# Kernel tuning notes

Measured on AMD Instinct MI355X. Metric: run time of the kernel, lower is better.

The kernel has to match this reference:

```python
import jax, jax.numpy as jnp
import numpy as np

FEAT_DIM = 128
NODE_DIM = 64
BS, C, H, W = 32, 128, 64, 64
TOPK = 4096


def setup_inputs() -> dict:
    key = jax.random.key(0)
    k1, k2, k3, k4, k5, k6 = jax.random.split(key, 6)
    feature_map = jax.random.normal(k1, (BS, C, H, W), dtype=jnp.float32)
    # peak (row, col) coordinates in heatmap/feature space, floats in-range
    rc = jax.random.uniform(k2, (BS, TOPK, 2), dtype=jnp.float32)
    peak_coords = rc * jnp.array([H - 1, W - 1], dtype=jnp.float32)
    s1 = 1.0 / np.sqrt(FEAT_DIM)
    s2 = 1.0 / np.sqrt(NODE_DIM)
    W1 = jax.random.uniform(k3, (FEAT_DIM, NODE_DIM), jnp.float32, -s1, s1)
    b1 = jax.random.uniform(k4, (NODE_DIM,), jnp.float32, -s1, s1)
    W2 = jax.random.uniform(k5, (NODE_DIM, NODE_DIM), jnp.float32, -s2, s2)
    b2 = jax.random.uniform(k6, (NODE_DIM,), jnp.float32, -s2, s2)
    return {"feature_map": feature_map, "peak_coords": peak_coords,
            "W1": W1, "b1": b1, "W2": W2, "b2": b2}


def _bilinear_gather(feature_map, peak_coords):
    # feature_map: (bs, C, H, W); peak_coords: (bs, topk, 2) as (row, col)
    # Equivalent to F.grid_sample(mode='bilinear', align_corners=True) at
    # grid built from coords normalized by (H-1)/(W-1): the normalization
    # round-trips, so we sample directly at pixel coords (y, x).
    bs, c, h, w = feature_map.shape
    fm = jnp.transpose(feature_map, (0, 2, 3, 1))  # (bs, H, W, C)
    y = peak_coords[..., 0]
    x = peak_coords[..., 1]
    y0 = jnp.floor(y)
    x0 = jnp.floor(x)
    ty = y - y0
    tx = x - x0
    y0i = jnp.clip(y0.astype(jnp.int32), 0, h - 1)
    x0i = jnp.clip(x0.astype(jnp.int32), 0, w - 1)
    y1i = jnp.clip(y0i + 1, 0, h - 1)
    x1i = jnp.clip(x0i + 1, 0, w - 1)
    b = jnp.arange(bs, dtype=jnp.int32)[:, None]  # (bs, 1)
    v00 = fm[b, y0i, x0i]  # (bs, topk, C)
    v01 = fm[b, y0i, x1i]
    v10 = fm[b, y1i, x0i]
    v11 = fm[b, y1i, x1i]
    ty = ty[..., None]
    tx = tx[..., None]
    top = v00 * (1 - tx) + v01 * tx
    bot = v10 * (1 - tx) + v11 * tx
    return top * (1 - ty) + bot * ty  # (bs, topk, C)


def reference(feature_map, peak_coords, W1, b1, W2, b2):
    sampled = _bilinear_gather(feature_map, peak_coords)  # (bs, topk, C)
    h = jax.nn.relu(jnp.einsum('btc,cd->btd', sampled, W1) + b1)
    e = jnp.einsum('btd,de->bte', h, W2) + b2  # (bs, topk, node_dim)
    norm = jnp.linalg.norm(e, axis=-1, keepdims=True)
    return e / jnp.maximum(norm, 1e-12)
```

## Files before the change

kernel.cpp:

```cpp
#include <hip/hip_runtime.h>

#define Hh 64
#define Ww 64
#define Cc 128
#define ND 64
#define BSz 32
#define TOPK 4096
#define HW (Hh * Ww)
#define NPX (BSz * HW)

typedef short bf16x8 __attribute__((ext_vector_type(8)));
typedef unsigned short u16x8 __attribute__((ext_vector_type(8)));
typedef float f32x4 __attribute__((ext_vector_type(4)));

static __device__ __forceinline__ unsigned short f2bf(float f) {
    unsigned int u = __builtin_bit_cast(unsigned int, f);
    u += 0x7fffu + ((u >> 16) & 1u);
    return (unsigned short)(u >> 16);
}
static __device__ __forceinline__ float bf2f(unsigned short s) {
    unsigned int u = ((unsigned int)s) << 16;
    return __builtin_bit_cast(float, u);
}

__global__ void k_prep(const float* __restrict__ W1, const float* __restrict__ W2,
                       unsigned short* __restrict__ w1p, unsigned short* __restrict__ w2p) {
    const int t = threadIdx.x;
#pragma unroll
    for (int k = 0; k < 32; ++k) {
        int i = t + 256 * k;
        int j = i & 7, l = (i >> 3) & 63, kk = (i >> 9) & 3, nt = i >> 11;
        int c = kk * 32 + 8 * (l >> 4) + j, n = nt * 16 + (l & 15);
        w1p[i] = f2bf(W1[c * ND + n]);
    }
#pragma unroll
    for (int k = 0; k < 16; ++k) {
        int i = t + 256 * k;
        int j = i & 7, l = (i >> 3) & 63, kk = (i >> 9) & 1, nt = (i >> 10) & 3;
        int c = kk * 32 + 8 * (l >> 4) + j, n = nt * 16 + (l & 15);
        w2p[i] = f2bf(W2[c * ND + n]);
    }
}

__global__ __launch_bounds__(256) void k_mlp1(const float* __restrict__ fm,
                                              const unsigned short* __restrict__ w1p,
                                              unsigned short* __restrict__ U) {
    __shared__ __align__(16) unsigned short w1s[8192];
    const int t = threadIdx.x;
#pragma unroll
    for (int k = 0; k < 4; ++k) {
        int i = t + 256 * k;
        *(u16x8*)&w1s[i * 8] = *(const u16x8*)&w1p[i * 8];
    }
    __syncthreads();

    const int bid = blockIdx.x;
    const int swz = (bid & 7) * 128 + (bid >> 3);
    const int lane = t & 63, wv = t >> 6;
    const int g = lane >> 4, mr = lane & 15;
    const int p0  = swz * 128 + wv * 32;
    const int b   = p0 >> 12;
    const int pin = p0 & 4095;
    const float* fb = fm + (size_t)b * (Cc * HW);

    bf16x8 aF[2][4];
#pragma unroll
    for (int half = 0; half < 2; ++half) {
        const int px = pin + half * 16 + mr;
#pragma unroll
        for (int kk = 0; kk < 4; ++kk) {
            float v[8];
#pragma unroll
            for (int j = 0; j < 8; ++j)
                v[j] = fb[(size_t)(kk * 32 + 8 * g + j) * HW + px];
            u16x8 o;
#pragma unroll
            for (int j = 0; j < 8; ++j) o[j] = f2bf(v[j]);
            aF[half][kk] = __builtin_bit_cast(bf16x8, o);
        }
    }

    f32x4 acc[2][4];
#pragma unroll
    for (int mt = 0; mt < 2; ++mt)
#pragma unroll
        for (int nt = 0; nt < 4; ++nt) acc[mt][nt] = (f32x4){0.f, 0.f, 0.f, 0.f};

#pragma unroll
    for (int kk = 0; kk < 4; ++kk)
#pragma unroll
        for (int nt = 0; nt < 4; ++nt) {
            bf16x8 bF = *(const bf16x8*)&w1s[((nt * 4 + kk) * 64 + lane) * 8];
            acc[0][nt] = __builtin_amdgcn_mfma_f32_16x16x32_bf16(aF[0][kk], bF, acc[0][nt], 0, 0, 0);
            acc[1][nt] = __builtin_amdgcn_mfma_f32_16x16x32_bf16(aF[1][kk], bF, acc[1][nt], 0, 0, 0);
        }

#pragma unroll
    for (int mt = 0; mt < 2; ++mt)
#pragma unroll
        for (int nt = 0; nt < 4; ++nt)
#pragma unroll
            for (int r = 0; r < 4; ++r) {
                const int row = p0 + mt * 16 + 4 * g + r;
                U[(size_t)row * ND + nt * 16 + mr] = f2bf(acc[mt][nt][r]);
            }
}

__global__ __launch_bounds__(256) void k_fused2(const unsigned short* __restrict__ U,
                                                const float* __restrict__ pc,
                                                const unsigned short* __restrict__ w2p,
                                                const float* __restrict__ b1,
                                                const float* __restrict__ b2,
                                                float* __restrict__ out) {
    __shared__ __align__(16) unsigned short w2s[4096];
    __shared__ __align__(16) float b1s[64];
    __shared__ __align__(16) float b2s[64];
    const int t = threadIdx.x;
#pragma unroll
    for (int k = 0; k < 2; ++k) {
        int i = t + 256 * k;
        *(u16x8*)&w2s[i * 8] = *(const u16x8*)&w2p[i * 8];
    }
    if (t < 64) { b1s[t] = b1[t]; b2s[t] = b2[t]; }
    __syncthreads();

    const int bid = blockIdx.x;
    const int swz = (bid & 7) * 256 + (bid >> 3);
    const int lane = t & 63, wv = t >> 6;
    const int g = lane >> 4, mr = lane & 15;
    const int m0 = swz * 64 + wv * 16;
    const int sm = m0 + mr;

    const float y = pc[2 * (size_t)sm + 0];
    const float x = pc[2 * (size_t)sm + 1];
    const float yf = floorf(y), xf = floorf(x);
    const float ty = y - yf, tx = x - xf;
    int y0 = min(max((int)yf, 0), Hh - 1);
    int x0 = min(max((int)xf, 0), Ww - 1);
    int y1 = min(y0 + 1, Hh - 1);
    int x1 = min(x0 + 1, Ww - 1);
    const float w00 = (1.f - ty) * (1.f - tx), w01 = (1.f - ty) * tx;
    const float w10 = ty * (1.f - tx),         w11 = ty * tx;
    const int bb = sm >> 12;
    const unsigned short* Ub = U + (size_t)bb * (HW * ND) + 8 * g;
    const u16x8* q00 = (const u16x8*)(Ub + (y0 * Ww + x0) * ND);
    const u16x8* q01 = (const u16x8*)(Ub + (y0 * Ww + x1) * ND);
    const u16x8* q10 = (const u16x8*)(Ub + (y1 * Ww + x0) * ND);
    const u16x8* q11 = (const u16x8*)(Ub + (y1 * Ww + x1) * ND);

    bf16x8 aF[2];
#pragma unroll
    for (int kk = 0; kk < 2; ++kk) {
        u16x8 a = q00[kk * 4], c0 = q01[kk * 4], c1 = q10[kk * 4], d = q11[kk * 4];
        f32x4 bA = *(const f32x4*)&b1s[kk * 32 + 8 * g];
        f32x4 bB = *(const f32x4*)&b1s[kk * 32 + 8 * g + 4];
        u16x8 o;
#pragma unroll
        for (int j = 0; j < 8; ++j) {
            float v = w00 * bf2f(a[j]) + w01 * bf2f(c0[j])
                    + w10 * bf2f(c1[j]) + w11 * bf2f(d[j]);
            float bv = (j < 4) ? bA[j & 3] : bB[j & 3];
            o[j] = f2bf(fmaxf(v + bv, 0.f));
        }
        aF[kk] = __builtin_bit_cast(bf16x8, o);
    }

    f32x4 acc2[4];
#pragma unroll
    for (int nt = 0; nt < 4; ++nt) {
        const float bc = b2s[nt * 16 + mr];
        acc2[nt] = (f32x4){bc, bc, bc, bc};
    }
#pragma unroll
    for (int kk = 0; kk < 2; ++kk)
#pragma unroll
        for (int nt = 0; nt < 4; ++nt) {
            bf16x8 bF = *(const bf16x8*)&w2s[((nt * 2 + kk) * 64 + lane) * 8];
            acc2[nt] = __builtin_amdgcn_mfma_f32_16x16x32_bf16(aF[kk], bF, acc2[nt], 0, 0, 0);
        }

    f32x4 ss = (f32x4){0.f, 0.f, 0.f, 0.f};
#pragma unroll
    for (int nt = 0; nt < 4; ++nt)
#pragma unroll
        for (int r = 0; r < 4; ++r) ss[r] += acc2[nt][r] * acc2[nt][r];
#pragma unroll
    for (int off = 1; off <= 8; off <<= 1) {
#pragma unroll
        for (int r = 0; r < 4; ++r) ss[r] += __shfl_xor(ss[r], off);
    }
#pragma unroll
    for (int r = 0; r < 4; ++r) {
        const float inv = 1.f / fmaxf(sqrtf(ss[r]), 1e-12f);
        const size_t ob = (size_t)(m0 + 4 * g + r) * ND;
#pragma unroll
        for (int nt = 0; nt < 4; ++nt)
            out[ob + nt * 16 + mr] = acc2[nt][r] * inv;
    }
}

extern "C" void kernel_launch(void* const* d_in, const int* in_sizes, int n_in,
                              void* d_out, int out_size, void* d_ws, size_t ws_size,
                              hipStream_t stream) {
    const float* fm = (const float*)d_in[0];
    const float* pc = (const float*)d_in[1];
    const float* W1 = (const float*)d_in[2];
    const float* b1 = (const float*)d_in[3];
    const float* W2 = (const float*)d_in[4];
    const float* b2 = (const float*)d_in[5];
    float* out = (float*)d_out;

    unsigned short* U   = (unsigned short*)d_ws;
    unsigned short* w1p = U + (size_t)NPX * ND;
    unsigned short* w2p = w1p + 8192;

    k_prep<<<1, 256, 0, stream>>>(W1, W2, w1p, w2p);
    k_mlp1<<<NPX / 128, 256, 0, stream>>>(fm, w1p, U);
    k_fused2<<<(BSz * TOPK) / 64, 256, 0, stream>>>(U, pc, w2p, b1, b2, out);
}
```

Before: 39.42 us.

## Fuse weight prep into consumer kernels and hoist bilinear corner loads

Result: slower. 42.68 us (+8.2%).

```diff
diff --git a/kernel.cpp b/kernel.cpp
--- a/kernel.cpp
+++ b/kernel.cpp
@@ -23,34 +23,17 @@
     return __builtin_bit_cast(float, u);
 }
 
-__global__ void k_prep(const float* __restrict__ W1, const float* __restrict__ W2,
-                       unsigned short* __restrict__ w1p, unsigned short* __restrict__ w2p) {
+__global__ __launch_bounds__(256) void k_mlp1(const float* __restrict__ fm,
+                                              const float* __restrict__ W1,
+                                              unsigned short* __restrict__ U) {
+    __shared__ __align__(16) unsigned short w1s[8192];
     const int t = threadIdx.x;
 #pragma unroll
     for (int k = 0; k < 32; ++k) {
         int i = t + 256 * k;
         int j = i & 7, l = (i >> 3) & 63, kk = (i >> 9) & 3, nt = i >> 11;
         int c = kk * 32 + 8 * (l >> 4) + j, n = nt * 16 + (l & 15);
-        w1p[i] = f2bf(W1[c * ND + n]);
-    }
-#pragma unroll
-    for (int k = 0; k < 16; ++k) {
-        int i = t + 256 * k;
-        int j = i & 7, l = (i >> 3) & 63, kk = (i >> 9) & 1, nt = (i >> 10) & 3;
-        int c = kk * 32 + 8 * (l >> 4) + j, n = nt * 16 + (l & 15);
-        w2p[i] = f2bf(W2[c * ND + n]);
-    }
-}
-
-__global__ __launch_bounds__(256) void k_mlp1(const float* __restrict__ fm,
-                                              const unsigned short* __restrict__ w1p,
-                                              unsigned short* __restrict__ U) {
-    __shared__ __align__(16) unsigned short w1s[8192];
-    const int t = threadIdx.x;
-#pragma unroll
-    for (int k = 0; k < 4; ++k) {
-        int i = t + 256 * k;
-        *(u16x8*)&w1s[i * 8] = *(const u16x8*)&w1p[i * 8];
+        w1s[i] = f2bf(W1[c * ND + n]);
     }
     __syncthreads();
 
@@ -108,7 +91,7 @@
 
 __global__ __launch_bounds__(256) void k_fused2(const unsigned short* __restrict__ U,
                                                 const float* __restrict__ pc,
-                                                const unsigned short* __restrict__ w2p,
+                                                const float* __restrict__ W2,
                                                 const float* __restrict__ b1,
                                                 const float* __restrict__ b2,
                                                 float* __restrict__ out) {
@@ -117,9 +100,11 @@
     __shared__ __align__(16) float b2s[64];
     const int t = threadIdx.x;
 #pragma unroll
-    for (int k = 0; k < 2; ++k) {
+    for (int k = 0; k < 16; ++k) {
         int i = t + 256 * k;
-        *(u16x8*)&w2s[i * 8] = *(const u16x8*)&w2p[i * 8];
+        int j = i & 7, l = (i >> 3) & 63, kk = (i >> 9) & 1, nt = (i >> 10) & 3;
+        int c = kk * 32 + 8 * (l >> 4) + j, n = nt * 16 + (l & 15);
+        w2s[i] = f2bf(W2[c * ND + n]);
     }
     if (t < 64) { b1s[t] = b1[t]; b2s[t] = b2[t]; }
     __syncthreads();
@@ -148,17 +133,25 @@
     const u16x8* q10 = (const u16x8*)(Ub + (y1 * Ww + x0) * ND);
     const u16x8* q11 = (const u16x8*)(Ub + (y1 * Ww + x1) * ND);
 
+    u16x8 r00[2], r01[2], r10[2], r11[2];
+#pragma unroll
+    for (int kk = 0; kk < 2; ++kk) {
+        r00[kk] = q00[kk * 4];
+        r01[kk] = q01[kk * 4];
+        r10[kk] = q10[kk * 4];
+        r11[kk] = q11[kk * 4];
+    }
+
     bf16x8 aF[2];
 #pragma unroll
     for (int kk = 0; kk < 2; ++kk) {
-        u16x8 a = q00[kk * 4], c0 = q01[kk * 4], c1 = q10[kk * 4], d = q11[kk * 4];
         f32x4 bA = *(const f32x4*)&b1s[kk * 32 + 8 * g];
         f32x4 bB = *(const f32x4*)&b1s[kk * 32 + 8 * g + 4];
         u16x8 o;
 #pragma unroll
         for (int j = 0; j < 8; ++j) {
-            float v = w00 * bf2f(a[j]) + w01 * bf2f(c0[j])
-                    + w10 * bf2f(c1[j]) + w11 * bf2f(d[j]);
+            float v = w00 * bf2f(r00[kk][j]) + w01 * bf2f(r01[kk][j])
+                    + w10 * bf2f(r10[kk][j]) + w11 * bf2f(r11[kk][j]);
             float bv = (j < 4) ? bA[j & 3] : bB[j & 3];
             o[j] = f2bf(fmaxf(v + bv, 0.f));
         }
@@ -210,11 +203,8 @@
     const float* b2 = (const float*)d_in[5];
     float* out = (float*)d_out;
 
-    unsigned short* U   = (unsigned short*)d_ws;
-    unsigned short* w1p = U + (size_t)NPX * ND;
-    unsigned short* w2p = w1p + 8192;
-
-    k_prep<<<1, 256, 0, stream>>>(W1, W2, w1p, w2p);
-    k_mlp1<<<NPX / 128, 256, 0, stream>>>(fm, w1p, U);
-    k_fused2<<<(BSz * TOPK) / 64, 256, 0, stream>>>(U, pc, w2p, b1, b2, out);
-}
+    unsigned short* U = (unsigned short*)d_ws;
+
+    k_mlp1<<<NPX / 128, 256, 0, stream>>>(fm, W1, U);
+    k_fused2<<<(BSz * TOPK) / 64, 256, 0, stream>>>(U, pc, W2, b1, b2, out);
+}
```
